# Performance work log

Hardware: AMD Instinct MI355X
Metric: run time of the kernel (lower is better)

Reference implementation:

```python
import jax, jax.numpy as jnp
import numpy as np

jax.config.update("jax_enable_x64", True)  # packing needs true int64 bit ops

_NORM12 = np.array([
    [3,1,1,1,3,3,3,3],[1,3,1,1,3,3,3,3],[1,1,3,1,3,3,3,3],[1,1,1,3,3,3,3,3],
    [3,3,3,1,3,3,1,1],[3,3,3,1,3,1,3,1],[3,3,3,1,1,3,3,1],[3,3,3,1,3,1,1,3],
    [3,3,3,1,1,3,1,3],[3,3,3,1,1,1,3,3],[3,3,1,3,3,3,1,1],[3,3,1,3,3,1,3,1],
    [3,3,1,3,1,3,3,1],[3,3,1,3,3,1,1,3],[3,3,1,3,1,3,1,3],[3,3,1,3,1,1,3,3],
    [3,1,3,3,3,3,1,1],[3,1,3,3,3,1,3,1],[3,1,3,3,1,3,3,1],[3,1,3,3,3,1,1,3],
    [3,1,3,3,1,3,1,3],[1,3,3,3,1,1,3,3],[1,3,3,3,3,3,1,1],[1,3,3,3,3,1,3,1],
    [1,3,3,3,1,3,3,1],[1,3,3,3,3,1,1,3],[1,3,3,3,1,3,1,3],[1,1,3,3,1,3,3,3],
    [3,3,1,1,3,3,3,1]], dtype=np.float32) / 2.0


def _build_packed_abs_grid():
    # faithful numpy port of get_packed_abs_grid()
    intr = np.arange(-4, 4)
    d8 = np.stack(np.meshgrid(*([intr] * 8), indexing='ij'), axis=-1).reshape(-1, 8).astype(np.float32) + 0.5
    mask = ((d8.sum(-1) % 2) == 0) & ((d8 * d8).sum(-1) <= 10)
    d8abs = np.unique(np.abs(d8[mask]), axis=0)
    cba = np.concatenate([d8abs, _NORM12], axis=0)          # [256, 8]
    cba = cba[:, [0, 2, 4, 6, 1, 3, 5, 7]]
    cba[:, 7] = cba[:, 7] * (1 - 2 * (cba.sum(1) % 2))
    cba = (cba * 2 + 8).astype(np.int64)
    acc = cba[:, 0].copy()
    for i in range(7):
        acc |= cba[:, i + 1] << ((i + 1) * 4)
    return acc                                              # [256] packed nibbles


def _build_full_grid(packed):
    # reconstruct the 2^16-entry E8P grid from the packed abs codewords
    SHUF = np.array([0, 4, 1, 5, 2, 6, 3, 7])               # inverse of [0,2,4,6,1,3,5,7]
    c = np.arange(1 << 16)
    signs = c & 255
    absi = c >> 8
    parity = (((signs[:, None] >> np.arange(8)) & 1).sum(1)) & 1
    signs = signs ^ parity
    nib = ((packed[absi][:, None] >> (4 * SHUF[None, :])) & 15).astype(np.float32)
    val = (nib - 8.0) / 2.0                                 # undo cba*2+8
    sbit = (signs[:, None] >> SHUF[None, :]) & 1
    val = np.where(sbit == 1, -val, val)
    val = val - 0.25 * parity[:, None].astype(np.float32)   # odd-parity coset shift
    return val.astype(np.float32)                           # [65536, 8]


def setup_inputs() -> dict:
    key = jax.random.key(0)
    packed = _build_packed_abs_grid()
    grid = jnp.asarray(_build_full_grid(packed))            # [65536, 8]
    grid_norm = (grid * grid).sum(-1)                       # [65536]
    X = jax.random.normal(key, (256, 32, 8), dtype=jnp.float32)
    return {"X": X, "grid": grid, "grid_norm": grid_norm}


def _pack_idxs(idxs):
    # faithful port of maybe_pack_idxs; idxs: int64 [m, n], m%16==0, n%8==0
    m, n = idxs.shape
    q = idxs.reshape(m // 2, 2, n // 2, 2).transpose(0, 2, 1, 3)   # [m//2, n//2, 2, 2]
    abs32 = ((q[:, :, 0, 0] >> 8)
             + ((q[:, :, 1, 0] >> 8) << 8)
             + ((q[:, :, 0, 1] >> 8) << 16)
             + ((q[:, :, 1, 1] >> 8) << 24))
    sign32 = jnp.zeros_like(abs32)
    for i in range(4):
        wt = q[:, :, i % 2, i // 2]
        for j in range(8):
            sign32 = sign32 + (((wt >> j) & 1) << (4 * j + i))
    out = (sign32 << 32) + abs32
    out = out.reshape(m // 16, 8, n // 8, 4).transpose(0, 2, 1, 3)
    return out.reshape(m, n // 4)


def reference(X, grid, grid_norm):
    m, n, _ = X.shape
    Xf = X.reshape(-1, 8)                                   # [m*n, 8]
    scores = 2.0 * (Xf @ grid.T) - grid_norm                # [m*n, 65536] (traffic-bound)
    idxs = jnp.argmax(scores, axis=-1).astype(jnp.int64)    # [m*n]
    vals = grid[idxs].reshape(m, n, 8)
    idxs = idxs.reshape(m, n)
    packed = _pack_idxs(idxs)                               # [m, n//4] int64
    return vals, idxs, packed
```

## Files before the change

### kernel.cpp

```cpp
#include <hip/hip_runtime.h>
#include <stdint.h>
#include <math.h>


__device__ __forceinline__ void cmp_keep(float& bs, int& bc, float s, int c) {
    if (s > bs || (s == bs && c < bc)) { bs = s; bc = c; }
}

__device__ __forceinline__ double pay_abs(double t, uint32_t pk16) {
    long long ll = __double_as_longlong(t) & 0x7FFFFFFFFFFF0000ll;
    return __longlong_as_double(ll | (long long)pk16);
}

struct TournOut { double a1c, a2c; uint32_t q1, q2; };

__device__ __forceinline__ TournOut tourn8(const double kk[8]) {
    double m01 = fmin(kk[0], kk[1]), x01 = fmax(kk[0], kk[1]);
    double m23 = fmin(kk[2], kk[3]), x23 = fmax(kk[2], kk[3]);
    double m45 = fmin(kk[4], kk[5]), x45 = fmax(kk[4], kk[5]);
    double m67 = fmin(kk[6], kk[7]), x67 = fmax(kk[6], kk[7]);
    double mA = fmin(m01, m23), sA = fmin(fmax(m01, m23), fmin(x01, x23));
    double mB = fmin(m45, m67), sB = fmin(fmax(m45, m67), fmin(x45, x67));
    double m1 = fmin(mA, mB),   m2 = fmin(fmax(mA, mB), fmin(sA, sB));
    long long b1 = __double_as_longlong(m1);
    long long b2 = __double_as_longlong(m2);
    TournOut o;
    o.a1c = __longlong_as_double(b1 & ~0xFFFFll);
    o.a2c = __longlong_as_double(b2 & ~0xFFFFll);
    o.q1 = (uint32_t)b1 & 0xFFFFu;
    o.q2 = (uint32_t)b2 & 0xFFFFu;
    return o;
}

__global__ __launch_bounds__(256) void e8p_fused3(
    const float* __restrict__ X,
    const float* __restrict__ grid,
    const float* __restrict__ grid_norm,
    float* __restrict__ out)
{
    __shared__ float2   sWp[4][256];
    __shared__ uint32_t sPK[4][256];
    __shared__ uint32_t sMeta[256];
    __shared__ float    sSN[256];
    __shared__ int      sC[4];

    const int tid = threadIdx.x;
    const int shuf[8] = {0, 4, 1, 5, 2, 6, 3, 7};

    {
        const float4* g4 = reinterpret_cast<const float4*>(grid + (size_t)tid * 2048);
        float4 lo = g4[0], hi = g4[1];
        float w[8] = {lo.x, lo.y, lo.z, lo.w, hi.x, hi.y, hi.z, hi.w};
        float aw[8]; uint32_t pk[8]; uint32_t wsgnshuf = 0;
#pragma unroll
        for (int j = 0; j < 8; ++j) {
            uint32_t sb = __float_as_uint(w[j]) >> 31;
            wsgnshuf |= sb << shuf[j];
            aw[j] = fabsf(w[j]);
            uint32_t tw = (uint32_t)(2.0f * aw[j]);
            pk[j] = (tw << 13) | ((uint32_t)j << 10) | (1u << shuf[j]);
        }
        sWp[0][tid] = make_float2(aw[0], aw[1]);
        sWp[1][tid] = make_float2(aw[2], aw[3]);
        sWp[2][tid] = make_float2(aw[4], aw[5]);
        sWp[3][tid] = make_float2(aw[6], aw[7]);
#pragma unroll
        for (int i = 0; i < 4; ++i) sPK[i][tid] = pk[2 * i] | (pk[2 * i + 1] << 16);
        sMeta[tid] = wsgnshuf | ((uint32_t)(__popc(wsgnshuf) & 1) << 8);
        sSN[tid] = grid_norm[(size_t)tid * 256];
    }
    __syncthreads();

    const int lane = tid & 63, wid = tid >> 6;
    const int A = blockIdx.x >> 4, B = blockIdx.x & 15;
    const int row = A * 64 + (wid >> 1) * 32 + B * 2 + (wid & 1);

    const float* xr = X + (size_t)row * 8;
    double xd[8], Sx = 0.0;
    uint32_t sp1b = 0, sp0sh = 0, sp1sh = 0, pp0 = 0, pp1 = 0;
#pragma unroll
    for (int j = 0; j < 8; ++j) {
        float xf = xr[j]; double d = (double)xf;
        xd[j] = d; Sx += d;
        uint32_t b0 = (xf < 0.0f) ? 1u : 0u;
        uint32_t b1 = (d < -0.25) ? 1u : 0u;
        sp1b |= b1 << j;
        sp0sh |= b0 << shuf[j]; sp1sh |= b1 << shuf[j];
        pp0 ^= b0; pp1 ^= b1;
    }

    float bestS = -INFINITY; int bestC = 0x7fffffff;

    for (int k = 0; k < 4; ++k) {
        const int absi = lane + (k << 6);
        float2 w01 = sWp[0][absi], w23 = sWp[1][absi], w45 = sWp[2][absi], w67 = sWp[3][absi];
        float awf[8] = {w01.x, w01.y, w23.x, w23.y, w45.x, w45.y, w67.x, w67.y};
        uint32_t pw0 = sPK[0][absi], pw1 = sPK[1][absi], pw2 = sPK[2][absi], pw3 = sPK[3][absi];
        uint32_t pk16[8] = {pw0 & 0xFFFFu, pw0 >> 16, pw1 & 0xFFFFu, pw1 >> 16,
                            pw2 & 0xFFFFu, pw2 >> 16, pw3 & 0xFFFFu, pw3 >> 16};
        const uint32_t meta = sMeta[absi];
        const float    sN   = sSN[absi];
        const uint32_t wsh = meta & 0xFFu, wpar = (meta >> 8) & 1u;

        double kk0[8], t1[8];
#pragma unroll
        for (int j = 0; j < 8; ++j) {
            double wd = (double)awf[j];
            double t0 = wd * xd[j];
            t1[j]  = fma(t0, 4.0, wd);
            kk0[j] = pay_abs(t0, pk16[j]);
        }

        {
            double Sab = ((fabs(kk0[0]) + fabs(kk0[1])) + (fabs(kk0[2]) + fabs(kk0[3])))
                       + ((fabs(kk0[4]) + fabs(kk0[5])) + (fabs(kk0[6]) + fabs(kk0[7])));
            TournOut o = tourn8(kk0);
            uint32_t sb1 = o.q1 & 0xFFu, sb2 = o.q2 & 0xFFu;
            uint32_t par = wpar ^ pp0;
            uint32_t seffb = wsh ^ sp0sh;
            double dA = par ? o.a1c : 0.0;
            double dB = par ? o.a2c : (o.a1c + o.a2c);
            uint32_t sbA = par ? sb1 : 0u;
            uint32_t sbB = par ? sb2 : (sb1 ^ sb2);
            { float f = (float)(Sab - 2.0 * dA);
              cmp_keep(bestS, bestC, 2.0f * f - sN, (absi << 8) | (int)(seffb ^ sbA)); }
            { float f = (float)(Sab - 2.0 * dB);
              cmp_keep(bestS, bestC, 2.0f * f - sN, (absi << 8) | (int)(seffb ^ sbB)); }
        }
        {
            double kk1[8];
#pragma unroll
            for (int j = 0; j < 8; ++j) kk1[j] = pay_abs(t1[j], pk16[j]);
            double Sab4 = ((fabs(kk1[0]) + fabs(kk1[1])) + (fabs(kk1[2]) + fabs(kk1[3])))
                        + ((fabs(kk1[4]) + fabs(kk1[5])) + (fabs(kk1[6]) + fabs(kk1[7])));
            TournOut o = tourn8(kk1);
            uint32_t sb1 = o.q1 & 0xFFu, sb2 = o.q2 & 0xFFu;
            uint32_t par = wpar ^ pp1;
            uint32_t seffb = wsh ^ sp1sh;
            double dA = par ? o.a1c : 0.0;
            double dB = par ? o.a2c : (o.a1c + o.a2c);
            uint32_t sbA = par ? sb1 : 0u;
            uint32_t sbB = par ? sb2 : (sb1 ^ sb2);
            float W0 = ((((sp1b >> 0) & 1) ? -awf[0] : awf[0]) + (((sp1b >> 1) & 1) ? -awf[1] : awf[1]))
                     + ((((sp1b >> 2) & 1) ? -awf[2] : awf[2]) + (((sp1b >> 3) & 1) ? -awf[3] : awf[3]))
                     + (((((sp1b >> 4) & 1) ? -awf[4] : awf[4]) + (((sp1b >> 5) & 1) ? -awf[5] : awf[5]))
                     +  ((((sp1b >> 6) & 1) ? -awf[6] : awf[6]) + (((sp1b >> 7) & 1) ? -awf[7] : awf[7])));
            uint32_t j1 = (o.q1 >> 10) & 7u, j2 = (o.q2 >> 10) & 7u;
            float w1f = 0.5f * (float)(o.q1 >> 13);
            float w2f = 0.5f * (float)(o.q2 >> 13);
            float sw1 = ((sp1b >> j1) & 1) ? -w1f : w1f;
            float sw2 = ((sp1b >> j2) & 1) ? -w2f : w2f;
            float swA = par ? sw1 : 0.0f;
            float swB = par ? sw2 : (sw1 + sw2);
            {
                float Wc = W0 - 2.0f * swA;
                double E = (Sab4 - 2.0 * dA) - ((double)Wc + Sx);
                float f = (float)(0.25 * E);
                float gnv = (sN - 0.5f * Wc) + 0.5f;
                cmp_keep(bestS, bestC, 2.0f * f - gnv,
                         (absi << 8) | (int)((seffb ^ sbA) ^ 1u));
            }
            {
                float Wc = W0 - 2.0f * swB;
                double E = (Sab4 - 2.0 * dB) - ((double)Wc + Sx);
                float f = (float)(0.25 * E);
                float gnv = (sN - 0.5f * Wc) + 0.5f;
                cmp_keep(bestS, bestC, 2.0f * f - gnv,
                         (absi << 8) | (int)((seffb ^ sbB) ^ 1u));
            }
        }
    }

#pragma unroll
    for (int off = 32; off > 0; off >>= 1) {
        float s2 = __shfl_xor(bestS, off);
        int   c2 = __shfl_xor(bestC, off);
        cmp_keep(bestS, bestC, s2, c2);
    }

    if (lane == 0) {
        const int c = bestC;
        const float4* gg = reinterpret_cast<const float4*>(grid + (size_t)c * 8);
        float4* v4 = reinterpret_cast<float4*>(out + (size_t)row * 8);
        v4[0] = gg[0]; v4[1] = gg[1];
        out[65536 + row] = (float)c;
        sC[wid] = c;
    }
    __syncthreads();

    if (tid == 0) {
        const uint32_t e00 = (uint32_t)sC[0], e01 = (uint32_t)sC[1];
        const uint32_t e10 = (uint32_t)sC[2], e11 = (uint32_t)sC[3];
        const uint32_t abs32 = (e00 >> 8) | ((e10 >> 8) << 8)
                             | ((e01 >> 8) << 16) | ((e11 >> 8) << 24);
        const int f = ((A >> 3) << 7) | ((B >> 2) << 5) | ((A & 7) << 2) | (B & 3);
        out[73728 + f] = (float)(int32_t)abs32;
    }
}

extern "C" void kernel_launch(void* const* d_in, const int* in_sizes, int n_in,
                              void* d_out, int out_size, void* d_ws, size_t ws_size,
                              hipStream_t stream)
{
    const float* X    = (const float*)d_in[0];
    const float* grid = (const float*)d_in[1];
    const float* gn   = (const float*)d_in[2];
    e8p_fused3<<<2048, 256, 0, stream>>>(X, grid, gn, (float*)d_out);
}
```

Measured before the change: 76.52 us.

## Screen candidates in fp32 and refine only near-best slots in fp64

```diff
diff --git a/kernel.cpp b/kernel.cpp
--- a/kernel.cpp
+++ b/kernel.cpp
@@ -3,13 +3,10 @@
 #include <math.h>
 
 
+#define EPS_SCREEN 2.0e-3f
+
 __device__ __forceinline__ void cmp_keep(float& bs, int& bc, float s, int c) {
     if (s > bs || (s == bs && c < bc)) { bs = s; bc = c; }
-}
-
-__device__ __forceinline__ double pay_abs(double t, uint32_t pk16) {
-    long long ll = __double_as_longlong(t) & 0x7FFFFFFFFFFF0000ll;
-    return __longlong_as_double(ll | (long long)pk16);
 }
 
 struct TournOut { double a1c, a2c; uint32_t q1, q2; };
@@ -32,7 +29,17 @@
     return o;
 }
 
-__global__ __launch_bounds__(256) void e8p_fused3(
+__device__ __forceinline__ float2 t8v(const float a[8]) {
+    float m01 = fminf(fabsf(a[0]), fabsf(a[1])), x01 = fmaxf(fabsf(a[0]), fabsf(a[1]));
+    float m23 = fminf(fabsf(a[2]), fabsf(a[3])), x23 = fmaxf(fabsf(a[2]), fabsf(a[3]));
+    float m45 = fminf(fabsf(a[4]), fabsf(a[5])), x45 = fmaxf(fabsf(a[4]), fabsf(a[5]));
+    float m67 = fminf(fabsf(a[6]), fabsf(a[7])), x67 = fmaxf(fabsf(a[6]), fabsf(a[7]));
+    float mA = fminf(m01, m23), sA = fminf(fmaxf(m01, m23), fminf(x01, x23));
+    float mB = fminf(m45, m67), sB = fminf(fmaxf(m45, m67), fminf(x45, x67));
+    return make_float2(fminf(mA, mB), fminf(fmaxf(mA, mB), fminf(sA, sB)));
+}
+
+__global__ __launch_bounds__(256) void e8p_screen(
     const float* __restrict__ X,
     const float* __restrict__ grid,
     const float* __restrict__ grid_norm,
@@ -76,71 +83,97 @@
     const int row = A * 64 + (wid >> 1) * 32 + B * 2 + (wid & 1);
 
     const float* xr = X + (size_t)row * 8;
-    double xd[8], Sx = 0.0;
+    float  xf[8]; double xd[8], Sx = 0.0;
     uint32_t sp1b = 0, sp0sh = 0, sp1sh = 0, pp0 = 0, pp1 = 0;
 #pragma unroll
     for (int j = 0; j < 8; ++j) {
-        float xf = xr[j]; double d = (double)xf;
-        xd[j] = d; Sx += d;
-        uint32_t b0 = (xf < 0.0f) ? 1u : 0u;
+        float f = xr[j]; double d = (double)f;
+        xf[j] = f; xd[j] = d; Sx += d;
+        uint32_t b0 = (f < 0.0f) ? 1u : 0u;
         uint32_t b1 = (d < -0.25) ? 1u : 0u;
         sp1b |= b1 << j;
         sp0sh |= b0 << shuf[j]; sp1sh |= b1 << shuf[j];
         pp0 ^= b0; pp1 ^= b1;
     }
-
-    float bestS = -INFINITY; int bestC = 0x7fffffff;
-
+    const float c1row = 0.5f * (float)Sx + 0.5f;
+
+    float apx[8];
+#pragma unroll
     for (int k = 0; k < 4; ++k) {
         const int absi = lane + (k << 6);
         float2 w01 = sWp[0][absi], w23 = sWp[1][absi], w45 = sWp[2][absi], w67 = sWp[3][absi];
         float awf[8] = {w01.x, w01.y, w23.x, w23.y, w45.x, w45.y, w67.x, w67.y};
-        uint32_t pw0 = sPK[0][absi], pw1 = sPK[1][absi], pw2 = sPK[2][absi], pw3 = sPK[3][absi];
-        uint32_t pk16[8] = {pw0 & 0xFFFFu, pw0 >> 16, pw1 & 0xFFFFu, pw1 >> 16,
-                            pw2 & 0xFFFFu, pw2 >> 16, pw3 & 0xFFFFu, pw3 >> 16};
-        const uint32_t meta = sMeta[absi];
-        const float    sN   = sSN[absi];
-        const uint32_t wsh = meta & 0xFFu, wpar = (meta >> 8) & 1u;
-
-        double kk0[8], t1[8];
-#pragma unroll
-        for (int j = 0; j < 8; ++j) {
-            double wd = (double)awf[j];
-            double t0 = wd * xd[j];
-            t1[j]  = fma(t0, 4.0, wd);
-            kk0[j] = pay_abs(t0, pk16[j]);
-        }
-
-        {
-            double Sab = ((fabs(kk0[0]) + fabs(kk0[1])) + (fabs(kk0[2]) + fabs(kk0[3])))
-                       + ((fabs(kk0[4]) + fabs(kk0[5])) + (fabs(kk0[6]) + fabs(kk0[7])));
-            TournOut o = tourn8(kk0);
+        const float sN = sSN[absi];
+        const uint32_t wpar = (sMeta[absi] >> 8) & 1u;
+        float t0s[8], t1s[8];
+#pragma unroll
+        for (int j = 0; j < 8; ++j) { t0s[j] = awf[j] * xf[j]; t1s[j] = fmaf(t0s[j], 4.0f, awf[j]); }
+        float S0 = ((fabsf(t0s[0]) + fabsf(t0s[1])) + (fabsf(t0s[2]) + fabsf(t0s[3])))
+                 + ((fabsf(t0s[4]) + fabsf(t0s[5])) + (fabsf(t0s[6]) + fabsf(t0s[7])));
+        float S4 = ((fabsf(t1s[0]) + fabsf(t1s[1])) + (fabsf(t1s[2]) + fabsf(t1s[3])))
+                 + ((fabsf(t1s[4]) + fabsf(t1s[5])) + (fabsf(t1s[6]) + fabsf(t1s[7])));
+        float2 mm0 = t8v(t0s);
+        float2 mm1 = t8v(t1s);
+        {   uint32_t par = wpar ^ pp0;
+            float dA = par ? mm0.x : 0.0f, dB = par ? mm0.y : (mm0.x + mm0.y);
+            float a = 2.0f * (S0 - 2.0f * dA) - sN;
+            float b = 2.0f * (S0 - 2.0f * dB) - sN;
+            apx[2 * k] = fmaxf(a, b); }
+        {   uint32_t par = wpar ^ pp1;
+            float dA = par ? mm1.x : 0.0f, dB = par ? mm1.y : (mm1.x + mm1.y);
+            float a = 0.5f * (S4 - 2.0f * dA) - sN - c1row;
+            float b = 0.5f * (S4 - 2.0f * dB) - sN - c1row;
+            apx[2 * k + 1] = fmaxf(a, b); }
+    }
+
+    float lm = apx[0];
+#pragma unroll
+    for (int i = 1; i < 8; ++i) lm = fmaxf(lm, apx[i]);
+    const float thr = lm - EPS_SCREEN;
+    uint32_t smask = 0;
+#pragma unroll
+    for (int i = 0; i < 8; ++i) smask |= (apx[i] >= thr ? 1u : 0u) << i;
+
+    float bestS = -INFINITY; int bestC = 0x7fffffff;
+
+    while (__any(smask != 0)) {
+        if (smask) {
+            const int slot = __ffs((int)smask) - 1;
+            smask &= smask - 1;
+            const int k = slot >> 1;
+            const uint32_t p = (uint32_t)(slot & 1);
+            const int absi = lane + (k << 6);
+
+            float2 w01 = sWp[0][absi], w23 = sWp[1][absi], w45 = sWp[2][absi], w67 = sWp[3][absi];
+            float awf[8] = {w01.x, w01.y, w23.x, w23.y, w45.x, w45.y, w67.x, w67.y};
+            uint32_t pw0 = sPK[0][absi], pw1 = sPK[1][absi], pw2 = sPK[2][absi], pw3 = sPK[3][absi];
+            uint32_t pk16[8] = {pw0 & 0xFFFFu, pw0 >> 16, pw1 & 0xFFFFu, pw1 >> 16,
+                                pw2 & 0xFFFFu, pw2 >> 16, pw3 & 0xFFFFu, pw3 >> 16};
+            const uint32_t meta = sMeta[absi];
+            const float    sN   = sSN[absi];
+            const uint32_t wsh = meta & 0xFFu, wpar = (meta >> 8) & 1u;
+
+            double kk[8];
+#pragma unroll
+            for (int j = 0; j < 8; ++j) {
+                double wd = (double)awf[j];
+                double t0 = wd * xd[j];
+                double tt = p ? fma(t0, 4.0, wd) : t0;
+                long long ll = __double_as_longlong(tt) & 0x7FFFFFFFFFFF0000ll;
+                kk[j] = __longlong_as_double(ll | (long long)pk16[j]);
+            }
+            double Sab = ((kk[0] + kk[1]) + (kk[2] + kk[3]))
+                       + ((kk[4] + kk[5]) + (kk[6] + kk[7]));
+
+            TournOut o = tourn8(kk);
             uint32_t sb1 = o.q1 & 0xFFu, sb2 = o.q2 & 0xFFu;
-            uint32_t par = wpar ^ pp0;
-            uint32_t seffb = wsh ^ sp0sh;
+            uint32_t par = wpar ^ (p ? pp1 : pp0);
+            uint32_t seffb = wsh ^ (p ? sp1sh : sp0sh);
             double dA = par ? o.a1c : 0.0;
             double dB = par ? o.a2c : (o.a1c + o.a2c);
             uint32_t sbA = par ? sb1 : 0u;
             uint32_t sbB = par ? sb2 : (sb1 ^ sb2);
-            { float f = (float)(Sab - 2.0 * dA);
-              cmp_keep(bestS, bestC, 2.0f * f - sN, (absi << 8) | (int)(seffb ^ sbA)); }
-            { float f = (float)(Sab - 2.0 * dB);
-              cmp_keep(bestS, bestC, 2.0f * f - sN, (absi << 8) | (int)(seffb ^ sbB)); }
-        }
-        {
-            double kk1[8];
-#pragma unroll
-            for (int j = 0; j < 8; ++j) kk1[j] = pay_abs(t1[j], pk16[j]);
-            double Sab4 = ((fabs(kk1[0]) + fabs(kk1[1])) + (fabs(kk1[2]) + fabs(kk1[3])))
-                        + ((fabs(kk1[4]) + fabs(kk1[5])) + (fabs(kk1[6]) + fabs(kk1[7])));
-            TournOut o = tourn8(kk1);
-            uint32_t sb1 = o.q1 & 0xFFu, sb2 = o.q2 & 0xFFu;
-            uint32_t par = wpar ^ pp1;
-            uint32_t seffb = wsh ^ sp1sh;
-            double dA = par ? o.a1c : 0.0;
-            double dB = par ? o.a2c : (o.a1c + o.a2c);
-            uint32_t sbA = par ? sb1 : 0u;
-            uint32_t sbB = par ? sb2 : (sb1 ^ sb2);
+
             float W0 = ((((sp1b >> 0) & 1) ? -awf[0] : awf[0]) + (((sp1b >> 1) & 1) ? -awf[1] : awf[1]))
                      + ((((sp1b >> 2) & 1) ? -awf[2] : awf[2]) + (((sp1b >> 3) & 1) ? -awf[3] : awf[3]))
                      + (((((sp1b >> 4) & 1) ? -awf[4] : awf[4]) + (((sp1b >> 5) & 1) ? -awf[5] : awf[5]))
@@ -152,22 +185,19 @@
             float sw2 = ((sp1b >> j2) & 1) ? -w2f : w2f;
             float swA = par ? sw1 : 0.0f;
             float swB = par ? sw2 : (sw1 + sw2);
-            {
-                float Wc = W0 - 2.0f * swA;
-                double E = (Sab4 - 2.0 * dA) - ((double)Wc + Sx);
-                float f = (float)(0.25 * E);
-                float gnv = (sN - 0.5f * Wc) + 0.5f;
-                cmp_keep(bestS, bestC, 2.0f * f - gnv,
-                         (absi << 8) | (int)((seffb ^ sbA) ^ 1u));
-            }
-            {
-                float Wc = W0 - 2.0f * swB;
-                double E = (Sab4 - 2.0 * dB) - ((double)Wc + Sx);
-                float f = (float)(0.25 * E);
-                float gnv = (sN - 0.5f * Wc) + 0.5f;
-                cmp_keep(bestS, bestC, 2.0f * f - gnv,
-                         (absi << 8) | (int)((seffb ^ sbB) ^ 1u));
-            }
+            float WcA = W0 - 2.0f * swA;
+            float WcB = W0 - 2.0f * swB;
+
+            {   double EA = (Sab - 2.0 * dA) - (p ? ((double)WcA + Sx) : 0.0);
+                float fA = (float)(p ? 0.25 * EA : EA);
+                float gnvA = p ? ((sN - 0.5f * WcA) + 0.5f) : sN;
+                cmp_keep(bestS, bestC, 2.0f * fA - gnvA,
+                         (absi << 8) | (int)(seffb ^ sbA ^ p)); }
+            {   double EB = (Sab - 2.0 * dB) - (p ? ((double)WcB + Sx) : 0.0);
+                float fB = (float)(p ? 0.25 * EB : EB);
+                float gnvB = p ? ((sN - 0.5f * WcB) + 0.5f) : sN;
+                cmp_keep(bestS, bestC, 2.0f * fB - gnvB,
+                         (absi << 8) | (int)(seffb ^ sbB ^ p)); }
         }
     }
 
@@ -205,5 +235,5 @@
     const float* X    = (const float*)d_in[0];
     const float* grid = (const float*)d_in[1];
     const float* gn   = (const float*)d_in[2];
-    e8p_fused3<<<2048, 256, 0, stream>>>(X, grid, gn, (float*)d_out);
-}
+    e8p_screen<<<2048, 256, 0, stream>>>(X, grid, gn, (float*)d_out);
+}
```

After: 71.35 us. 6.8% less time.
